# Kernel optimization log

Measured on AMD Instinct MI355X. Metric: run time of the kernel, lower is better.

Reference implementation:

```python
import jax, jax.numpy as jnp
import numpy as np

LAYER_SIZES = [256, 256, 256]
SPLIT_HALF = True
B, F0, D = 512, 32, 32


def setup_inputs() -> dict:
    key = jax.random.key(0)
    ks = jax.random.split(key, 7)
    field_nums = [F0]
    for i, s in enumerate(LAYER_SIZES):
        field_nums.append(s // 2 if (SPLIT_HALF and i != len(LAYER_SIZES) - 1) else (s // 2 if SPLIT_HALF else s))
    # field_nums = [32, 128, 128, 128] (last entry unused for weights)
    inp = {
        'feat': jax.random.normal(ks[0], (B, F0, D), dtype=jnp.float32),
        'W0': jax.random.normal(ks[1], (LAYER_SIZES[0], field_nums[0], F0), dtype=jnp.float32) * 0.05,
        'b0': jnp.zeros((LAYER_SIZES[0],), dtype=jnp.float32),
        'W1': jax.random.normal(ks[2], (LAYER_SIZES[1], field_nums[1], F0), dtype=jnp.float32) * 0.05,
        'b1': jnp.zeros((LAYER_SIZES[1],), dtype=jnp.float32),
        'W2': jax.random.normal(ks[3], (LAYER_SIZES[2], field_nums[2], F0), dtype=jnp.float32) * 0.05,
        'b2': jnp.zeros((LAYER_SIZES[2],), dtype=jnp.float32),
    }
    return inp


def _cin_layer(h, feat, W, b):
    # h: [B,H,D], feat: [B,F0,D], W: [K,H,F0], b: [K] -> out [B,K,D]
    # outer product per embedding dim, then 1x1 conv (full [H,F0] contraction)
    z = jnp.einsum('bid,bjd->bdij', h, feat)          # [B,D,H,F0]
    out = jnp.einsum('bdij,kij->bkd', z, W) + b[None, :, None]
    return jax.nn.relu(out)


def reference(feat, W0, b0, W1, b1, W2, b2):
    Ws = [W0, W1, W2]
    bs = [b0, b1, b2]
    h = feat
    p = []
    n_layers = len(LAYER_SIZES)
    for l, K in enumerate(LAYER_SIZES):
        out = _cin_layer(h, feat, Ws[l], bs[l])        # [B,K,D]
        if SPLIT_HALF and l != n_layers - 1:
            h = out[:, :K // 2, :]
            direct = out[:, K // 2:, :]
        else:
            direct = out
            h = out
        p.append(direct)
    return jnp.concatenate(p, axis=1).sum(-1)          # [B, sum of direct sizes]
```

## Files before the change

### kernel.cpp

```cpp
#include <hip/hip_runtime.h>
#include <hip/hip_fp16.h>
#include <stdint.h>


typedef _Float16 half8_t __attribute__((ext_vector_type(8)));
typedef float f32x4 __attribute__((ext_vector_type(4)));
typedef float f32x16 __attribute__((ext_vector_type(16)));
typedef uint32_t u32x4 __attribute__((ext_vector_type(4)));

union H8 {
  half8_t h;
  uint32_t u[4];
  u32x4 q;
};

#define AS1 __attribute__((address_space(1)))
#define AS3 __attribute__((address_space(3)))

static __device__ __forceinline__ uint32_t pkmul(uint32_t x, uint32_t y) {
  __half2 a = __builtin_bit_cast(__half2, x);
  __half2 b = __builtin_bit_cast(__half2, y);
  __half2 r = __hmul2(a, b);
  return __builtin_bit_cast(uint32_t, r);
}

static __device__ __forceinline__ uint32_t pack2h(float a, float b) {
  __half2 r = __floats2half2_rn(a, b);
  return __builtin_bit_cast(uint32_t, r);
}

__global__ void prep_kernel(const float* __restrict__ W0, const float* __restrict__ W1,
                            const float* __restrict__ W2, const float* __restrict__ feat,
                            uint16_t* __restrict__ Wt0, uint16_t* __restrict__ Wt1,
                            uint16_t* __restrict__ Wt2,
                            uint16_t* __restrict__ F16, uint32_t* __restrict__ hP0) {
  int blk = blockIdx.x;
  if (blk < 4608) {
    const float* W; uint16_t* Wt; int FLsh, base;
    if (blk < 512)       { W = W0; Wt = Wt0; FLsh = 5; base = 0; }
    else if (blk < 2560) { W = W1; Wt = Wt1; FLsh = 7; base = 512; }
    else                 { W = W2; Wt = Wt2; FLsh = 7; base = 2560; }
    int idx2 = (blk - base) * 256 + threadIdx.x;
    float2 xy = *(const float2*)(W + (size_t)idx2 * 2);
    int j2 = idx2 & 15;
    int i = (idx2 >> 4) & ((1 << FLsh) - 1);
    int k = idx2 >> (4 + FLsh);
    __half2 h2 = __floats2half2_rn(xy.x, xy.y);
    int g = j2 >> 2, kr = k & 15, kt = k >> 4;
    uint32_t* wt32 = (uint32_t*)Wt;
    wt32[(((size_t)i * 16 + kt) * 64 + g * 16 + kr) * 4 + (j2 & 3)] = *(uint32_t*)&h2;
  } else {
    int m = (blk - 4608) * 256 + threadIdx.x;
    int b = m >> 5, d = m & 31;
    const float* fb = feat + (size_t)b * 1024 + d;
    uint16_t hs[32];
#pragma unroll
    for (int j = 0; j < 32; ++j)
      hs[j] = __half_as_ushort(__float2half(fb[j * 32]));
    int mb = m >> 5, ml = m & 31;
#pragma unroll
    for (int jp = 0; jp < 16; ++jp) {
      uint32_t pr = (uint32_t)hs[2 * jp] | ((uint32_t)hs[2 * jp + 1] << 16);
      hP0[((size_t)(mb * 4 + (jp >> 2)) * 4 + (jp & 3)) * 32 + ml] = pr;
    }
#pragma unroll
    for (int c = 0; c < 4; ++c) {
      u32x4 q;
      q[0] = (uint32_t)hs[c * 8 + 0] | ((uint32_t)hs[c * 8 + 1] << 16);
      q[1] = (uint32_t)hs[c * 8 + 2] | ((uint32_t)hs[c * 8 + 3] << 16);
      q[2] = (uint32_t)hs[c * 8 + 4] | ((uint32_t)hs[c * 8 + 5] << 16);
      q[3] = (uint32_t)hs[c * 8 + 6] | ((uint32_t)hs[c * 8 + 7] << 16);
      *(u32x4*)(F16 + (size_t)m * 32 + c * 8) = q;
    }
  }
}

template <int FL>
__global__ __launch_bounds__(256) void gemm_cin(
    const uint32_t* __restrict__ hP,
    const uint16_t* __restrict__ wt,
    const uint16_t* __restrict__ f16m,
    const float* __restrict__ bias,
    uint32_t* __restrict__ houtP,
    float* __restrict__ outp,
    int obase, int klo) {
  constexpr int NCH = FL / 16;
  __shared__ __align__(16) char smem[65536];
  const int tid = threadIdx.x;
  const int lane = tid & 63, w = tid >> 6;
  const int l31 = lane & 31, l5 = lane >> 5;
  const int kg = blockIdx.x & 7, mgrp = blockIdx.x >> 3;
  const int mb0 = mgrp * 8 + w * 2;

  const char* wsrc = (const char*)wt + kg * 2048 + (size_t)(tid >> 7) * 16384 +
                     (tid & 127) * 16;
  char* sdst = smem + tid * 16;

#define STAGE(Q)                                                              \
  { _Pragma("unroll") for (int c_ = 0; c_ < 8; ++c_)                          \
      __builtin_amdgcn_global_load_lds(                                       \
          (const AS1 uint32_t*)(wsrc + (size_t)((Q) * 16 + c_ * 2) * 16384),  \
          (AS3 uint32_t*)(sdst + ((Q) & 1) * 32768 + c_ * 4096), 16, 0, 0); }

  const uint32_t* hbA = hP + (size_t)mb0 * (FL / 8) * 128 + l31;
  const uint32_t* hbB = hbA + (size_t)(FL / 8) * 128;

#define HLD(HB, Q, G, DST)                                                    \
  { const uint32_t* p_ = (HB) + ((Q) * 2 + (G)) * 128;                        \
    DST[0] = p_[0]; DST[1] = p_[32]; DST[2] = p_[64]; DST[3] = p_[96]; }

  STAGE(0)
  if (NCH > 1) STAGE(1)
  u32x4 hA0, hA1, hB0, hB1, nA0, nA1, nB0, nB1;
  HLD(hbA, 0, 0, hA0) HLD(hbA, 0, 1, hA1)
  HLD(hbB, 0, 0, hB0) HLD(hbB, 0, 1, hB1)

  const uint16_t* fb0 = f16m + (size_t)(mb0 * 32 + l31) * 32 + l5 * 8;
  H8 ffA0, ffA1, ffB0, ffB1;
  ffA0.q = *(const u32x4*)(fb0);
  ffA1.q = *(const u32x4*)(fb0 + 16);
  ffB0.q = *(const u32x4*)(fb0 + 1024);
  ffB1.q = *(const u32x4*)(fb0 + 1040);

  f32x16 accA = {}, accB = {};
  const char* rb = smem + ((l31 >> 4) << 10) + (l5 << 8) + ((lane & 15) << 4);

  asm volatile("s_waitcnt vmcnt(0)" ::: "memory");
  asm volatile("s_barrier" ::: "memory");

#define CSTEP(S, HCA, HCB, RBQ)                                                    \
  {                                                                                \
    uint32_t hA_ = HCA[((S) >> 1) & 3], hB_ = HCB[((S) >> 1) & 3];                 \
    uint32_t sel_ = ((S) & 1) ? 0x03020302u : 0x01000100u;                         \
    uint32_t eA_ = __builtin_amdgcn_perm(hA_, hA_, sel_);                          \
    uint32_t eB_ = __builtin_amdgcn_perm(hB_, hB_, sel_);                          \
    H8 wf0_, wf1_, bA0_, bA1_, bB0_, bB1_;                                         \
    wf0_.q = *(const u32x4*)((RBQ) + (S) * 2048);                                  \
    wf1_.q = *(const u32x4*)((RBQ) + (S) * 2048 + 512);                            \
    _Pragma("unroll") for (int c_ = 0; c_ < 4; ++c_) {                             \
      bA0_.u[c_] = pkmul(ffA0.u[c_], eA_);                                         \
      bA1_.u[c_] = pkmul(ffA1.u[c_], eA_);                                         \
      bB0_.u[c_] = pkmul(ffB0.u[c_], eB_);                                         \
      bB1_.u[c_] = pkmul(ffB1.u[c_], eB_);                                         \
    }                                                                              \
    accA = __builtin_amdgcn_mfma_f32_32x32x16_f16(wf0_.h, bA0_.h, accA, 0, 0, 0);  \
    accA = __builtin_amdgcn_mfma_f32_32x32x16_f16(wf1_.h, bA1_.h, accA, 0, 0, 0);  \
    accB = __builtin_amdgcn_mfma_f32_32x32x16_f16(wf0_.h, bB0_.h, accB, 0, 0, 0);  \
    accB = __builtin_amdgcn_mfma_f32_32x32x16_f16(wf1_.h, bB1_.h, accB, 0, 0, 0);  \
  }

#define CHUNK(Q, CA0, CA1, CB0, CB1, NA0_, NA1_, NB0_, NB1_)                  \
  {                                                                           \
    const char* rbq_ = rb + ((Q) & 1) * 32768;                                \
    CSTEP(0, CA0, CB0, rbq_) CSTEP(1, CA0, CB0, rbq_)                         \
    if ((Q) + 1 < NCH) {                                                      \
      HLD(hbA, (Q) + 1, 0, NA0_) HLD(hbA, (Q) + 1, 1, NA1_)                   \
      HLD(hbB, (Q) + 1, 0, NB0_) HLD(hbB, (Q) + 1, 1, NB1_)                   \
    }                                                                         \
    CSTEP(2, CA0, CB0, rbq_) CSTEP(3, CA0, CB0, rbq_)                         \
    CSTEP(4, CA0, CB0, rbq_) CSTEP(5, CA0, CB0, rbq_)                         \
    CSTEP(6, CA0, CB0, rbq_) CSTEP(7, CA0, CB0, rbq_)                         \
    CSTEP(8, CA1, CB1, rbq_) CSTEP(9, CA1, CB1, rbq_)                         \
    CSTEP(10, CA1, CB1, rbq_) CSTEP(11, CA1, CB1, rbq_)                       \
    CSTEP(12, CA1, CB1, rbq_) CSTEP(13, CA1, CB1, rbq_)                       \
    CSTEP(14, CA1, CB1, rbq_) CSTEP(15, CA1, CB1, rbq_)                       \
  }

#define BOUNDARY(QS)                                                          \
  {                                                                           \
    asm volatile("s_waitcnt vmcnt(0)" ::: "memory");                          \
    asm volatile("s_barrier" ::: "memory");                                   \
    if ((QS) < NCH) STAGE(QS)                                                 \
  }

#pragma unroll 1
  for (int qq = 0; qq < NCH; qq += 2) {
    CHUNK(qq, hA0, hA1, hB0, hB1, nA0, nA1, nB0, nB1)
    BOUNDARY(qq + 2)
    CHUNK(qq + 1, nA0, nA1, nB0, nB1, hA0, hA1, hB0, hB1)
    if (qq + 2 < NCH) BOUNDARY(qq + 3)
  }
#undef CHUNK
#undef CSTEP
#undef BOUNDARY
#undef STAGE
#undef HLD

  f32x4 bv[4];
#pragma unroll
  for (int a = 0; a < 4; ++a)
    bv[a] = *(const f32x4*)(bias + kg * 32 + a * 8 + l5 * 4);

#define EPILOG(ACC, MB)                                                           \
  {                                                                               \
    float v[16];                                                                  \
    _Pragma("unroll") for (int a = 0; a < 4; ++a)                                 \
        _Pragma("unroll") for (int t = 0; t < 4; ++t) {                           \
      float x = ACC[a * 4 + t] + bv[a][t];                                        \
      v[a * 4 + t] = x > 0.f ? x : 0.f;                                           \
    }                                                                             \
    if (houtP != nullptr && kg < 4) {                                             \
      _Pragma("unroll") for (int a = 0; a < 4; ++a)                               \
          _Pragma("unroll") for (int c = 0; c < 2; ++c) {                         \
        uint32_t pr = pack2h(v[a * 4 + 2 * c], v[a * 4 + 2 * c + 1]);             \
        houtP[((size_t)((MB) * 16 + kg * 4 + a) * 4 + 2 * l5 + c) * 32 + l31] =   \
            pr;                                                                   \
      }                                                                           \
    }                                                                             \
    _Pragma("unroll") for (int r = 0; r < 16; ++r) {                              \
      float x = v[r];                                                             \
      x += __shfl_xor(x, 1); x += __shfl_xor(x, 2);                               \
      x += __shfl_xor(x, 4); x += __shfl_xor(x, 8);                               \
      x += __shfl_xor(x, 16);                                                     \
      v[r] = x;                                                                   \
    }                                                                             \
    if (kg * 32 >= klo && (lane == 0 || lane == 32)) {                            \
      float* ob = outp + (size_t)(MB) * 512 + obase + kg * 32 - klo + l5 * 4;     \
      _Pragma("unroll") for (int a = 0; a < 4; ++a)                               \
          *(f32x4*)(ob + a * 8) =                                                 \
              (f32x4){v[a * 4], v[a * 4 + 1], v[a * 4 + 2], v[a * 4 + 3]};        \
    }                                                                             \
  }

  EPILOG(accA, mb0)
  EPILOG(accB, mb0 + 1)
#undef EPILOG
}

extern "C" void kernel_launch(void* const* d_in, const int* in_sizes, int n_in,
                              void* d_out, int out_size, void* d_ws, size_t ws_size,
                              hipStream_t stream) {
  const float* feat = (const float*)d_in[0];
  const float* W0 = (const float*)d_in[1];
  const float* b0 = (const float*)d_in[2];
  const float* W1 = (const float*)d_in[3];
  const float* b1 = (const float*)d_in[4];
  const float* W2 = (const float*)d_in[5];
  const float* b2 = (const float*)d_in[6];
  float* out = (float*)d_out;
  char* ws = (char*)d_ws;

  uint16_t* Wt0 = (uint16_t*)(ws + 0x000000);
  uint16_t* Wt1 = (uint16_t*)(ws + 0x080000);
  uint16_t* Wt2 = (uint16_t*)(ws + 0x280000);
  uint16_t* F16 = (uint16_t*)(ws + 0x480000);
  uint32_t* hP0 = (uint32_t*)(ws + 0x580000);
  uint32_t* hP1 = (uint32_t*)(ws + 0x680000);
  uint32_t* hP2 = (uint32_t*)(ws + 0xA80000);

  prep_kernel<<<4672, 256, 0, stream>>>(W0, W1, W2, feat, Wt0, Wt1, Wt2, F16, hP0);

  gemm_cin<32><<<512, 256, 0, stream>>>(hP0, Wt0, F16, b0, hP1, out, 0, 128);
  gemm_cin<128><<<512, 256, 0, stream>>>(hP1, Wt1, F16, b1, hP2, out, 128, 128);
  gemm_cin<128><<<512, 256, 0, stream>>>(hP2, Wt2, F16, b2, (uint32_t*)nullptr,
                                         out, 256, 0);
}
```

Before: 95.34 us.

## Triple-buffer weight staging with smaller chunks and vectorize weight prep

The GEMM main loop moves from two 32KB LDS buffers of 16 sub-steps each to a rotating three-buffer ring of 16KB chunks. Prefetch is issued two chunks ahead with partial vmcnt waits, one barrier per chunk, all LDS weight fragments loaded before the MFMAs, and s_setprio raised around the MFMA bursts. The prep kernel now has each thread convert eight weights with float4 loads and one 16-byte store, so it launches about a quarter as many blocks. The aim is better load/compute overlap and less barrier stall, at the cost of more registers and redundant wrap-around prefetches of the last chunks.

```diff
diff --git a/kernel.cpp b/kernel.cpp
--- a/kernel.cpp
+++ b/kernel.cpp
@@ -35,22 +35,27 @@
                             uint16_t* __restrict__ Wt2,
                             uint16_t* __restrict__ F16, uint32_t* __restrict__ hP0) {
   int blk = blockIdx.x;
-  if (blk < 4608) {
+  if (blk < 1152) {
     const float* W; uint16_t* Wt; int FLsh, base;
-    if (blk < 512)       { W = W0; Wt = Wt0; FLsh = 5; base = 0; }
-    else if (blk < 2560) { W = W1; Wt = Wt1; FLsh = 7; base = 512; }
-    else                 { W = W2; Wt = Wt2; FLsh = 7; base = 2560; }
-    int idx2 = (blk - base) * 256 + threadIdx.x;
-    float2 xy = *(const float2*)(W + (size_t)idx2 * 2);
-    int j2 = idx2 & 15;
-    int i = (idx2 >> 4) & ((1 << FLsh) - 1);
-    int k = idx2 >> (4 + FLsh);
-    __half2 h2 = __floats2half2_rn(xy.x, xy.y);
-    int g = j2 >> 2, kr = k & 15, kt = k >> 4;
-    uint32_t* wt32 = (uint32_t*)Wt;
-    wt32[(((size_t)i * 16 + kt) * 64 + g * 16 + kr) * 4 + (j2 & 3)] = *(uint32_t*)&h2;
+    if (blk < 128)      { W = W0; Wt = Wt0; FLsh = 5; base = 0; }
+    else if (blk < 640) { W = W1; Wt = Wt1; FLsh = 7; base = 128; }
+    else                { W = W2; Wt = Wt2; FLsh = 7; base = 640; }
+    int idx4 = (blk - base) * 256 + threadIdx.x;
+    int jg = idx4 & 3;
+    int i = (idx4 >> 2) & ((1 << FLsh) - 1);
+    int k = idx4 >> (2 + FLsh);
+    const float* src = W + ((size_t)(k << FLsh) + i) * 32 + jg * 8;
+    float4 x0 = *(const float4*)(src);
+    float4 x1 = *(const float4*)(src + 4);
+    u32x4 o;
+    o[0] = pack2h(x0.x, x0.y);
+    o[1] = pack2h(x0.z, x0.w);
+    o[2] = pack2h(x1.x, x1.y);
+    o[3] = pack2h(x1.z, x1.w);
+    int kr = k & 15, kt = k >> 4;
+    *(u32x4*)((uint32_t*)Wt + (((size_t)i * 16 + kt) * 64 + jg * 16 + kr) * 4) = o;
   } else {
-    int m = (blk - 4608) * 256 + threadIdx.x;
+    int m = (blk - 1152) * 256 + threadIdx.x;
     int b = m >> 5, d = m & 31;
     const float* fb = feat + (size_t)b * 1024 + d;
     uint16_t hs[32];
@@ -84,36 +89,14 @@
     uint32_t* __restrict__ houtP,
     float* __restrict__ outp,
     int obase, int klo) {
-  constexpr int NCH = FL / 16;
-  __shared__ __align__(16) char smem[65536];
+  constexpr int NCHK = FL / 8;
+  constexpr int NCM = NCHK - 1;
+  __shared__ __align__(16) char smem[49152];
   const int tid = threadIdx.x;
   const int lane = tid & 63, w = tid >> 6;
   const int l31 = lane & 31, l5 = lane >> 5;
   const int kg = blockIdx.x & 7, mgrp = blockIdx.x >> 3;
   const int mb0 = mgrp * 8 + w * 2;
-
-  const char* wsrc = (const char*)wt + kg * 2048 + (size_t)(tid >> 7) * 16384 +
-                     (tid & 127) * 16;
-  char* sdst = smem + tid * 16;
-
-#define STAGE(Q)                                                              \
-  { _Pragma("unroll") for (int c_ = 0; c_ < 8; ++c_)                          \
-      __builtin_amdgcn_global_load_lds(                                       \
-          (const AS1 uint32_t*)(wsrc + (size_t)((Q) * 16 + c_ * 2) * 16384),  \
-          (AS3 uint32_t*)(sdst + ((Q) & 1) * 32768 + c_ * 4096), 16, 0, 0); }
-
-  const uint32_t* hbA = hP + (size_t)mb0 * (FL / 8) * 128 + l31;
-  const uint32_t* hbB = hbA + (size_t)(FL / 8) * 128;
-
-#define HLD(HB, Q, G, DST)                                                    \
-  { const uint32_t* p_ = (HB) + ((Q) * 2 + (G)) * 128;                        \
-    DST[0] = p_[0]; DST[1] = p_[32]; DST[2] = p_[64]; DST[3] = p_[96]; }
-
-  STAGE(0)
-  if (NCH > 1) STAGE(1)
-  u32x4 hA0, hA1, hB0, hB1, nA0, nA1, nB0, nB1;
-  HLD(hbA, 0, 0, hA0) HLD(hbA, 0, 1, hA1)
-  HLD(hbB, 0, 0, hB0) HLD(hbB, 0, 1, hB1)
 
   const uint16_t* fb0 = f16m + (size_t)(mb0 * 32 + l31) * 32 + l5 * 8;
   H8 ffA0, ffA1, ffB0, ffB1;
@@ -122,69 +105,104 @@
   ffB0.q = *(const u32x4*)(fb0 + 1024);
   ffB1.q = *(const u32x4*)(fb0 + 1040);
 
+  const char* wsrc = (const char*)wt + kg * 2048 + (size_t)(tid >> 7) * 16384 +
+                     (tid & 127) * 16;
+  char* sdst = smem + tid * 16;
+
+#define STAGE(QQ, BUFOFF)                                                     \
+  { const char* s_ = wsrc + (size_t)((QQ) & NCM) * 131072;                    \
+    char* d_ = sdst + (BUFOFF);                                               \
+    _Pragma("unroll") for (int c_ = 0; c_ < 4; ++c_)                          \
+      __builtin_amdgcn_global_load_lds(                                       \
+          (const AS1 uint32_t*)(s_ + c_ * 32768),                             \
+          (AS3 uint32_t*)(d_ + c_ * 4096), 16, 0, 0); }
+
+  const uint32_t* hbA = hP + (size_t)mb0 * (FL / 8) * 128 + l31;
+  const uint32_t* hbB = hbA + (size_t)(FL / 8) * 128;
+
+#define HLD(QQ, DA, DB)                                                       \
+  { const uint32_t* pa_ = hbA + ((QQ) & NCM) * 128;                           \
+    const uint32_t* pb_ = hbB + ((QQ) & NCM) * 128;                           \
+    DA[0] = pa_[0]; DA[1] = pa_[32]; DA[2] = pa_[64]; DA[3] = pa_[96];        \
+    DB[0] = pb_[0]; DB[1] = pb_[32]; DB[2] = pb_[64]; DB[3] = pb_[96]; }
+
+  u32x4 hcA, hcB, hnA, hnB;
+
+  STAGE(0, 0)
+  STAGE(1, 16384)
+  HLD(0, hcA, hcB)
+
   f32x16 accA = {}, accB = {};
-  const char* rb = smem + ((l31 >> 4) << 10) + (l5 << 8) + ((lane & 15) << 4);
-
-  asm volatile("s_waitcnt vmcnt(0)" ::: "memory");
-  asm volatile("s_barrier" ::: "memory");
-
-#define CSTEP(S, HCA, HCB, RBQ)                                                    \
-  {                                                                                \
-    uint32_t hA_ = HCA[((S) >> 1) & 3], hB_ = HCB[((S) >> 1) & 3];                 \
-    uint32_t sel_ = ((S) & 1) ? 0x03020302u : 0x01000100u;                         \
-    uint32_t eA_ = __builtin_amdgcn_perm(hA_, hA_, sel_);                          \
-    uint32_t eB_ = __builtin_amdgcn_perm(hB_, hB_, sel_);                          \
-    H8 wf0_, wf1_, bA0_, bA1_, bB0_, bB1_;                                         \
-    wf0_.q = *(const u32x4*)((RBQ) + (S) * 2048);                                  \
-    wf1_.q = *(const u32x4*)((RBQ) + (S) * 2048 + 512);                            \
-    _Pragma("unroll") for (int c_ = 0; c_ < 4; ++c_) {                             \
-      bA0_.u[c_] = pkmul(ffA0.u[c_], eA_);                                         \
-      bA1_.u[c_] = pkmul(ffA1.u[c_], eA_);                                         \
-      bB0_.u[c_] = pkmul(ffB0.u[c_], eB_);                                         \
-      bB1_.u[c_] = pkmul(ffB1.u[c_], eB_);                                         \
-    }                                                                              \
-    accA = __builtin_amdgcn_mfma_f32_32x32x16_f16(wf0_.h, bA0_.h, accA, 0, 0, 0);  \
-    accA = __builtin_amdgcn_mfma_f32_32x32x16_f16(wf1_.h, bA1_.h, accA, 0, 0, 0);  \
-    accB = __builtin_amdgcn_mfma_f32_32x32x16_f16(wf0_.h, bB0_.h, accB, 0, 0, 0);  \
-    accB = __builtin_amdgcn_mfma_f32_32x32x16_f16(wf1_.h, bB1_.h, accB, 0, 0, 0);  \
-  }
-
-#define CHUNK(Q, CA0, CA1, CB0, CB1, NA0_, NA1_, NB0_, NB1_)                  \
-  {                                                                           \
-    const char* rbq_ = rb + ((Q) & 1) * 32768;                                \
-    CSTEP(0, CA0, CB0, rbq_) CSTEP(1, CA0, CB0, rbq_)                         \
-    if ((Q) + 1 < NCH) {                                                      \
-      HLD(hbA, (Q) + 1, 0, NA0_) HLD(hbA, (Q) + 1, 1, NA1_)                   \
-      HLD(hbB, (Q) + 1, 0, NB0_) HLD(hbB, (Q) + 1, 1, NB1_)                   \
-    }                                                                         \
-    CSTEP(2, CA0, CB0, rbq_) CSTEP(3, CA0, CB0, rbq_)                         \
-    CSTEP(4, CA0, CB0, rbq_) CSTEP(5, CA0, CB0, rbq_)                         \
-    CSTEP(6, CA0, CB0, rbq_) CSTEP(7, CA0, CB0, rbq_)                         \
-    CSTEP(8, CA1, CB1, rbq_) CSTEP(9, CA1, CB1, rbq_)                         \
-    CSTEP(10, CA1, CB1, rbq_) CSTEP(11, CA1, CB1, rbq_)                       \
-    CSTEP(12, CA1, CB1, rbq_) CSTEP(13, CA1, CB1, rbq_)                       \
-    CSTEP(14, CA1, CB1, rbq_) CSTEP(15, CA1, CB1, rbq_)                       \
-  }
-
-#define BOUNDARY(QS)                                                          \
-  {                                                                           \
-    asm volatile("s_waitcnt vmcnt(0)" ::: "memory");                          \
-    asm volatile("s_barrier" ::: "memory");                                   \
-    if ((QS) < NCH) STAGE(QS)                                                 \
-  }
-
+  const char* rbase = smem + ((l31 >> 4) << 10) + (l5 << 8) + ((lane & 15) << 4);
+
+  asm volatile("s_waitcnt vmcnt(12)" ::: "memory");
+  __builtin_amdgcn_s_barrier();
+
+#define MSTEP(W0_, W1_, HA_, HB_, PSEL)                                           \
+  { uint32_t eA_ = __builtin_amdgcn_perm((HA_), (HA_), (PSEL));                   \
+    uint32_t eB_ = __builtin_amdgcn_perm((HB_), (HB_), (PSEL));                   \
+    H8 bA0_, bA1_, bB0_, bB1_;                                                    \
+    _Pragma("unroll") for (int c_ = 0; c_ < 4; ++c_) {                            \
+      bA0_.u[c_] = pkmul(ffA0.u[c_], eA_);                                        \
+      bA1_.u[c_] = pkmul(ffA1.u[c_], eA_);                                        \
+      bB0_.u[c_] = pkmul(ffB0.u[c_], eB_);                                        \
+      bB1_.u[c_] = pkmul(ffB1.u[c_], eB_);                                        \
+    }                                                                             \
+    accA = __builtin_amdgcn_mfma_f32_32x32x16_f16((W0_).h, bA0_.h, accA, 0, 0, 0); \
+    accA = __builtin_amdgcn_mfma_f32_32x32x16_f16((W1_).h, bA1_.h, accA, 0, 0, 0); \
+    accB = __builtin_amdgcn_mfma_f32_32x32x16_f16((W0_).h, bB0_.h, accB, 0, 0, 0); \
+    accB = __builtin_amdgcn_mfma_f32_32x32x16_f16((W1_).h, bB1_.h, accB, 0, 0, 0); }
+
+#define CHUNK(QQ, RDOFF, STOFF, HCA_, HCB_, HNA_, HNB_)                           \
+  { const char* rb_ = rbase + (RDOFF);                                            \
+    H8 w0, w1, w2, w3, w4, w5, w6, w7, w8, w9, wa, wb, wc, wd, we, wf;            \
+    w0.q = *(const u32x4*)(rb_ + 0 * 2048);                                       \
+    w1.q = *(const u32x4*)(rb_ + 0 * 2048 + 512);                                 \
+    w2.q = *(const u32x4*)(rb_ + 1 * 2048);                                       \
+    w3.q = *(const u32x4*)(rb_ + 1 * 2048 + 512);                                 \
+    w4.q = *(const u32x4*)(rb_ + 2 * 2048);                                       \
+    w5.q = *(const u32x4*)(rb_ + 2 * 2048 + 512);                                 \
+    w6.q = *(const u32x4*)(rb_ + 3 * 2048);                                       \
+    w7.q = *(const u32x4*)(rb_ + 3 * 2048 + 512);                                 \
+    HLD((QQ) + 1, HNA_, HNB_)                                                     \
+    STAGE((QQ) + 2, STOFF)                                                        \
+    w8.q = *(const u32x4*)(rb_ + 4 * 2048);                                       \
+    w9.q = *(const u32x4*)(rb_ + 4 * 2048 + 512);                                 \
+    wa.q = *(const u32x4*)(rb_ + 5 * 2048);                                       \
+    wb.q = *(const u32x4*)(rb_ + 5 * 2048 + 512);                                 \
+    wc.q = *(const u32x4*)(rb_ + 6 * 2048);                                       \
+    wd.q = *(const u32x4*)(rb_ + 6 * 2048 + 512);                                 \
+    we.q = *(const u32x4*)(rb_ + 7 * 2048);                                       \
+    wf.q = *(const u32x4*)(rb_ + 7 * 2048 + 512);                                 \
+    __builtin_amdgcn_s_setprio(1);                                                \
+    MSTEP(w0, w1, HCA_[0], HCB_[0], 0x01000100u)                                  \
+    MSTEP(w2, w3, HCA_[0], HCB_[0], 0x03020302u)                                  \
+    MSTEP(w4, w5, HCA_[1], HCB_[1], 0x01000100u)                                  \
+    MSTEP(w6, w7, HCA_[1], HCB_[1], 0x03020302u)                                  \
+    __builtin_amdgcn_s_setprio(0);                                                \
+    __builtin_amdgcn_s_setprio(1);                                                \
+    MSTEP(w8, w9, HCA_[2], HCB_[2], 0x01000100u)                                  \
+    MSTEP(wa, wb, HCA_[2], HCB_[2], 0x03020302u)                                  \
+    MSTEP(wc, wd, HCA_[3], HCB_[3], 0x01000100u)                                  \
+    MSTEP(we, wf, HCA_[3], HCB_[3], 0x03020302u)                                  \
+    __builtin_amdgcn_s_setprio(0);                                                \
+    asm volatile("s_waitcnt vmcnt(12)" ::: "memory");                             \
+    __builtin_amdgcn_s_barrier();                                                 \
+  }
+
+  int r0 = 0, r1 = 16384, r2 = 32768;
 #pragma unroll 1
-  for (int qq = 0; qq < NCH; qq += 2) {
-    CHUNK(qq, hA0, hA1, hB0, hB1, nA0, nA1, nB0, nB1)
-    BOUNDARY(qq + 2)
-    CHUNK(qq + 1, nA0, nA1, nB0, nB1, hA0, hA1, hB0, hB1)
-    if (qq + 2 < NCH) BOUNDARY(qq + 3)
+  for (int q = 0; q < NCHK; q += 2) {
+    CHUNK(q, r0, r2, hcA, hcB, hnA, hnB)
+    CHUNK(q + 1, r1, r0, hnA, hnB, hcA, hcB)
+    int t = r2; r2 = r1; r1 = r0; r0 = t;
   }
 #undef CHUNK
-#undef CSTEP
-#undef BOUNDARY
+#undef MSTEP
 #undef STAGE
 #undef HLD
+
+  asm volatile("s_waitcnt vmcnt(0)" ::: "memory");
 
   f32x4 bv[4];
 #pragma unroll
@@ -248,7 +266,7 @@
   uint32_t* hP1 = (uint32_t*)(ws + 0x680000);
   uint32_t* hP2 = (uint32_t*)(ws + 0xA80000);
 
-  prep_kernel<<<4672, 256, 0, stream>>>(W0, W1, W2, feat, Wt0, Wt1, Wt2, F16, hP0);
+  prep_kernel<<<1216, 256, 0, stream>>>(W0, W1, W2, feat, Wt0, Wt1, Wt2, F16, hP0);
 
   gemm_cin<32><<<512, 256, 0, stream>>>(hP0, Wt0, F16, b0, hP1, out, 0, 128);
   gemm_cin<128><<<512, 256, 0, stream>>>(hP1, Wt1, F16, b1, hP2, out, 128, 128);
```

New measurement: 96.94 us. No clear change (+1.7%).
